# Performance work log

Measured on AMD Instinct MI355X. Metric: run time of the kernel, lower is better.

Reference implementation:

```python
import jax, jax.numpy as jnp
import numpy as np

DIM = 4096
HEADS = 32
HD = DIM // HEADS  # 128
SEQ = 2048
BSZ = 2
ALEN = 10
ROPE_THETA = 10000.0


def _make_freqs(seq, hd):
    inv = 1.0 / (ROPE_THETA ** (np.arange(0, hd, 2, dtype=np.float32) / hd))
    t = np.arange(seq, dtype=np.float32)
    ang = np.outer(t, inv)  # [seq, hd/2]
    return jnp.asarray(np.cos(ang)), jnp.asarray(np.sin(ang))


def setup_inputs() -> dict:
    key = jax.random.key(0)
    ks = jax.random.split(key, 8)
    s = 1.0 / np.sqrt(DIM)
    x = jax.random.normal(ks[0], (BSZ, SEQ, DIM), jnp.float32)
    wq = jax.random.normal(ks[1], (DIM, DIM), jnp.float32) * s  # [in, out]
    wk = jax.random.normal(ks[2], (DIM, DIM), jnp.float32) * s
    wv = jax.random.normal(ks[3], (DIM, DIM), jnp.float32) * s
    wo = jax.random.normal(ks[4], (DIM, DIM), jnp.float32) * s
    gate = 0.1 * jax.random.normal(ks[5], (1, HEADS, 1, 1), jnp.float32)
    adapter = jax.random.normal(ks[6], (1, ALEN, DIM), jnp.float32)
    freqs_cos, freqs_sin = _make_freqs(SEQ, HD)
    # causal additive mask, start_pos = 0
    mask = jnp.triu(jnp.full((1, 1, SEQ, SEQ), -1e9, jnp.float32), k=1)
    return {"x": x, "wq": wq, "wk": wk, "wv": wv, "wo": wo, "gate": gate,
            "adapter": adapter, "freqs_cos": freqs_cos, "freqs_sin": freqs_sin,
            "mask": mask, "start_pos": 0, "random_init": 0}


def _rope(t, cos, sin):
    # t: [b, s, H, hd]; cos/sin: [s, hd/2] -> broadcast (1, s, 1, hd/2)
    b, s, h, hd = t.shape
    t2 = t.reshape(b, s, h, hd // 2, 2)
    tr, ti = t2[..., 0], t2[..., 1]
    c = cos[None, :, None, :]
    sn = sin[None, :, None, :]
    orr = tr * c - ti * sn
    oi = tr * sn + ti * c
    return jnp.stack([orr, oi], axis=-1).reshape(b, s, h, hd)


def reference(x, wq, wk, wv, wo, gate, adapter, freqs_cos, freqs_sin, mask,
              start_pos, random_init):
    bsz, seqlen, dim = x.shape
    hd = 2 * freqs_cos.shape[-1]
    H = dim // hd
    L = adapter.shape[1]
    scale = 1.0 / jnp.sqrt(jnp.float32(hd))

    xq = (x @ wq).reshape(bsz, seqlen, H, hd)
    xk = (x @ wk).reshape(bsz, seqlen, H, hd)
    xv = (x @ wv).reshape(bsz, seqlen, H, hd)

    xq = _rope(xq, freqs_cos, freqs_sin)
    xk = _rope(xk, freqs_cos, freqs_sin)

    # adapter prefix K/V (no RoPE), shared across batch
    ak = (adapter @ wk).reshape(1, L, H, hd)  # [1, L, H, hd]
    av = (adapter @ wv).reshape(1, L, H, hd)

    # scores: normal keys masked causally; adapter keys unmasked (extra zeros)
    scores_n = jnp.einsum('bqhd,bkhd->bhqk', xq, xk) * scale + mask
    scores_a = jnp.einsum('bqhd,lhd->bhql', xq, ak[0]) * scale

    if random_init:
        # joint softmax over [adapter | normal] keys
        sc = jax.nn.softmax(jnp.concatenate([scores_a, scores_n], axis=-1), axis=-1)
        pa, pn = sc[..., :L], sc[..., L:]
    else:
        pa = jnp.tanh(gate) * jax.nn.softmax(scores_a, axis=-1)
        pn = jax.nn.softmax(scores_n, axis=-1)

    out = (jnp.einsum('bhql,lhd->bqhd', pa, av[0])
           + jnp.einsum('bhqk,bkhd->bqhd', pn, xv))
    out = out.reshape(bsz, seqlen, H * hd)
    return out @ wo
```

## Files before the change

### kernel.cpp

```cpp
#include <hip/hip_runtime.h>
#include <hip/hip_bf16.h>
#include <cstdint>

typedef float  f32x4  __attribute__((ext_vector_type(4)));
typedef __bf16 bf16x8 __attribute__((ext_vector_type(8)));
typedef __bf16 bf16x4 __attribute__((ext_vector_type(4)));
typedef __bf16 bf16x2 __attribute__((ext_vector_type(2)));

#define AS1 __attribute__((address_space(1)))
#define AS3 __attribute__((address_space(3)))

static constexpr int D   = 4096;
static constexpr int SEQ = 2048;
static constexpr int MX  = 4224;

__device__ __forceinline__ void gload_lds16(const void* g, void* l) {
  __builtin_amdgcn_global_load_lds((AS1 void*)(g), (AS3 void*)(l), 16, 0, 0);
}

__device__ __forceinline__ f32x4 mfma16(bf16x8 a, bf16x8 b, f32x4 c) {
  return __builtin_amdgcn_mfma_f32_16x16x32_bf16(a, b, c, 0, 0, 0);
}

__device__ __forceinline__ int xcd_chunk(int orig, int nwg) {
  int q = nwg >> 3, r = nwg & 7;
  int xcd = orig & 7, pos = orig >> 3;
  return (xcd < r ? xcd * (q + 1) : r * (q + 1) + (xcd - r) * q) + pos;
}

#define BARF() asm volatile("s_barrier" ::: "memory")

__global__ __launch_bounds__(256) void transpose_cast(const float* __restrict__ W,
                                                      __bf16* __restrict__ WT) {
  __shared__ float tile[64][65];
  const int t  = threadIdx.x;
  const int r0 = blockIdx.x * 64;
  const int c0 = blockIdx.y * 64;
#pragma unroll
  for (int p = 0; p < 4; ++p) {
    int e = p * 1024 + t * 4;
    int row = e >> 6, col = e & 63;
    f32x4 v = *(const f32x4*)(W + (size_t)(r0 + row) * D + c0 + col);
#pragma unroll
    for (int i = 0; i < 4; ++i) tile[row][col + i] = v[i];
  }
  __syncthreads();
#pragma unroll
  for (int p = 0; p < 2; ++p) {
    int e = p * 2048 + t * 8;
    int orow = e >> 6, ocol = e & 63;
    bf16x8 o;
#pragma unroll
    for (int i = 0; i < 8; ++i) o[i] = (__bf16)tile[ocol + i][orow];
    *(bf16x8*)(WT + (size_t)(c0 + orow) * D + r0 + ocol) = o;
  }
}

__global__ __launch_bounds__(256) void build_xa(const float* __restrict__ x,
                                                const float* __restrict__ ad,
                                                __bf16* __restrict__ xa) {
  int idx = blockIdx.x * 256 + threadIdx.x;
  int e = idx * 4;
  int row = e >> 12, col = e & 4095;
  f32x4 v = {};
  if (row < 4096)      v = *(const f32x4*)(x + (size_t)row * D + col);
  else if (row < 4106) v = *(const f32x4*)(ad + (size_t)(row - 4096) * D + col);
  bf16x4 o;
#pragma unroll
  for (int i = 0; i < 4; ++i) o[i] = (__bf16)v[i];
  *(bf16x4*)(xa + (size_t)row * D + col) = o;
}

template <int MODE>
__global__ __launch_bounds__(512, 2) void gemm256(const __bf16* __restrict__ A,
                                                  const __bf16* __restrict__ BT,
                                                  void* __restrict__ O0,
                                                  void* __restrict__ O1,
                                                  void* __restrict__ O2,
                                                  int Mt) {
  __shared__ __bf16 lds[65536];
  const int tid = threadIdx.x;
  const int wv = tid >> 6, ln = tid & 63;
  const int lg = ln >> 4, lr = ln & 15;

  const int nwg = gridDim.x;
  const int wgid = xcd_chunk(blockIdx.x, nwg);
  const int m0 = (wgid % Mt) * 256;
  const int n0 = (wgid / Mt) * 256;

  const int wm = (wv >> 2) * 128, wn = (wv & 3) * 64;

  auto stage = [&](int t) {
    const int buf = t & 1;
    const int kt = t * 64;
#pragma unroll
    for (int i = 0; i < 8; ++i) {
      int c = i * 512 + tid;
      int mat = c >> 11;
      int cm = c & 2047;
      int r = cm >> 3;
      int ch = (cm & 7) ^ (r & 7);
      const __bf16* src = mat ? (BT + (size_t)(n0 + r) * 4096 + kt + ch * 8)
                              : (A  + (size_t)(m0 + r) * 4096 + kt + ch * 8);
      int base = buf * 32768 + mat * 16384 + ((i * 512 + wv * 64) & 2047) * 8;
      gload_lds16(src, lds + base);
    }
  };

  f32x4 acc[8][4] = {};
  bf16x8 aLo[4][2], aHi[4][2], bLo[2][2], bHi[2][2];

  stage(0);

  for (int t = 0; t < 64; ++t) {
    const int buf = t & 1;
    if (t + 1 < 64) {
      stage(t + 1);
      asm volatile("s_waitcnt vmcnt(8)" ::: "memory");
    } else {
      asm volatile("s_waitcnt vmcnt(0)" ::: "memory");
    }
    BARF();

    const __bf16* pA = lds + buf * 32768;
    const __bf16* pB = lds + buf * 32768 + 16384;

    auto rdA = [&](int mi, int kk) -> bf16x8 {
      int r = wm + mi * 16 + lr;
      int R = r & 127;
      int cw = (kk * 4 + lg) ^ (R & 7);
      return *(const bf16x8*)(pA + (r >> 7) * 8192 + R * 64 + cw * 8);
    };
    auto rdB = [&](int ni, int kk) -> bf16x8 {
      int n = wn + ni * 16 + lr;
      int R = n & 127;
      int cw = (kk * 4 + lg) ^ (R & 7);
      return *(const bf16x8*)(pB + (n >> 7) * 8192 + R * 64 + cw * 8);
    };

#pragma unroll
    for (int mi = 0; mi < 4; ++mi)
#pragma unroll
      for (int kk = 0; kk < 2; ++kk) aLo[mi][kk] = rdA(mi, kk);
#pragma unroll
    for (int ni = 0; ni < 2; ++ni)
#pragma unroll
      for (int kk = 0; kk < 2; ++kk) bLo[ni][kk] = rdB(ni, kk);
    BARF();
    __builtin_amdgcn_s_setprio(1);
#pragma unroll
    for (int kk = 0; kk < 2; ++kk)
#pragma unroll
      for (int mi = 0; mi < 4; ++mi)
#pragma unroll
        for (int ni = 0; ni < 2; ++ni)
          acc[mi][ni] = mfma16(aLo[mi][kk], bLo[ni][kk], acc[mi][ni]);
    __builtin_amdgcn_s_setprio(0);

#pragma unroll
    for (int mi = 0; mi < 4; ++mi)
#pragma unroll
      for (int kk = 0; kk < 2; ++kk) aHi[mi][kk] = rdA(mi + 4, kk);
    BARF();
    __builtin_amdgcn_s_setprio(1);
#pragma unroll
    for (int kk = 0; kk < 2; ++kk)
#pragma unroll
      for (int mi = 0; mi < 4; ++mi)
#pragma unroll
        for (int ni = 0; ni < 2; ++ni)
          acc[mi + 4][ni] = mfma16(aHi[mi][kk], bLo[ni][kk], acc[mi + 4][ni]);
    __builtin_amdgcn_s_setprio(0);

#pragma unroll
    for (int ni = 0; ni < 2; ++ni)
#pragma unroll
      for (int kk = 0; kk < 2; ++kk) bHi[ni][kk] = rdB(ni + 2, kk);
    BARF();
    __builtin_amdgcn_s_setprio(1);
#pragma unroll
    for (int kk = 0; kk < 2; ++kk)
#pragma unroll
      for (int mi = 0; mi < 4; ++mi)
#pragma unroll
        for (int ni = 0; ni < 2; ++ni)
          acc[mi + 4][ni + 2] = mfma16(aHi[mi][kk], bHi[ni][kk], acc[mi + 4][ni + 2]);
    __builtin_amdgcn_s_setprio(0);

#pragma unroll
    for (int mi = 0; mi < 4; ++mi)
#pragma unroll
      for (int kk = 0; kk < 2; ++kk) aLo[mi][kk] = rdA(mi, kk);
    BARF();
    __builtin_amdgcn_s_setprio(1);
#pragma unroll
    for (int kk = 0; kk < 2; ++kk)
#pragma unroll
      for (int mi = 0; mi < 4; ++mi)
#pragma unroll
        for (int ni = 0; ni < 2; ++ni)
          acc[mi][ni + 2] = mfma16(aLo[mi][kk], bHi[ni][kk], acc[mi][ni + 2]);
    __builtin_amdgcn_s_setprio(0);

    BARF();
  }

  if constexpr (MODE == 0) {
    const int sel = n0 >> 12;
    __bf16* out = (sel == 0) ? (__bf16*)O0 : (sel == 1) ? (__bf16*)O1 : (__bf16*)O2;
    const int colb = n0 & 4095;
    const int Mmax = (sel == 0) ? 4096 : 4224;
#pragma unroll
    for (int mi = 0; mi < 8; ++mi)
#pragma unroll
      for (int j = 0; j < 4; ++j) {
        int row = m0 + wm + mi * 16 + lg * 4 + j;
        if (row < Mmax) {
#pragma unroll
          for (int ni = 0; ni < 4; ++ni) {
            int col = colb + wn + ni * 16 + lr;
            out[(size_t)row * 4096 + col] = (__bf16)acc[mi][ni][j];
          }
        }
      }
  } else {
    float* out = (float*)O0;
#pragma unroll
    for (int mi = 0; mi < 8; ++mi)
#pragma unroll
      for (int ni = 0; ni < 4; ++ni)
#pragma unroll
        for (int j = 0; j < 4; ++j) {
          int row = m0 + wm + mi * 16 + lg * 4 + j;
          int col = n0 + wn + ni * 16 + lr;
          out[(size_t)row * 4096 + col] = acc[mi][ni][j];
        }
  }
}

__global__ __launch_bounds__(256) void rope_kernel(__bf16* __restrict__ q,
                                                   __bf16* __restrict__ k,
                                                   const float* __restrict__ fc,
                                                   const float* __restrict__ fs) {
  int row = blockIdx.x;
  __bf16* buf = blockIdx.y ? k : q;
  int t = threadIdx.x;
  int s = row & (SEQ - 1);
  int jb = (t & 7) * 8;
  const float* cp = fc + s * 64 + jb;
  const float* sp = fs + s * 64 + jb;
  __bf16* p = buf + (size_t)row * D + t * 16;
  bf16x8 v0 = *(const bf16x8*)p;
  bf16x8 v1 = *(const bf16x8*)(p + 8);
  bf16x8 o0, o1;
#pragma unroll
  for (int i = 0; i < 4; ++i) {
    float C = cp[i], Sn = sp[i];
    float re = (float)v0[2 * i], im = (float)v0[2 * i + 1];
    o0[2 * i]     = (__bf16)(re * C - im * Sn);
    o0[2 * i + 1] = (__bf16)(re * Sn + im * C);
  }
#pragma unroll
  for (int i = 0; i < 4; ++i) {
    float C = cp[4 + i], Sn = sp[4 + i];
    float re = (float)v1[2 * i], im = (float)v1[2 * i + 1];
    o1[2 * i]     = (__bf16)(re * C - im * Sn);
    o1[2 * i + 1] = (__bf16)(re * Sn + im * C);
  }
  *(bf16x8*)p = o0;
  *(bf16x8*)(p + 8) = o1;
}

__global__ __launch_bounds__(256) void transpose_v(const __bf16* __restrict__ V,
                                                   __bf16* __restrict__ VT) {
  __shared__ __bf16 tile[64][72];
  const int t  = threadIdx.x;
  const int r0 = blockIdx.x * 64;
  const int c0 = blockIdx.y * 64;
#pragma unroll
  for (int p = 0; p < 2; ++p) {
    int e = p * 2048 + t * 8;
    int row = e >> 6, col = e & 63;
    bf16x8 v8 = *(const bf16x8*)(V + (size_t)(r0 + row) * D + c0 + col);
#pragma unroll
    for (int i = 0; i < 8; ++i) tile[row][col + i] = v8[i];
  }
  __syncthreads();
#pragma unroll
  for (int p = 0; p < 2; ++p) {
    int e = p * 2048 + t * 8;
    int orow = e >> 6, ocol = e & 63;
    bf16x8 o;
#pragma unroll
    for (int i = 0; i < 8; ++i) o[i] = tile[ocol + i][orow];
    *(bf16x8*)(VT + (size_t)(c0 + orow) * MX + r0 + ocol) = o;
  }
}

__global__ __launch_bounds__(256) void attn_kernel(const __bf16* __restrict__ Q,
                                                   const __bf16* __restrict__ K,
                                                   const __bf16* __restrict__ VT,
                                                   const float* __restrict__ gate,
                                                   __bf16* __restrict__ Out) {
  __shared__ __bf16 Ks[2][64 * 128];
  __shared__ __bf16 Vs[2][128 * 64];
  __shared__ __bf16 Ps[4][32 * 64];

  const int tid = threadIdx.x;
  const int wv = tid >> 6, ln = tid & 63;
  const int lg = ln >> 4, lr = ln & 15;

  const int wgid = xcd_chunk(blockIdx.x, 512);
  const int px = wgid & 7;
  const int hb = wgid >> 3;
  const int h = hb & 31, b = hb >> 5;

  const float scale = 0.08838834764831845f;
  const float g = tanhf(gate[h]);

  auto stage = [&](int t, int buf) {
    const int kv0 = t * 64;
#pragma unroll
    for (int j = 0; j < 4; ++j) {
      int c = wv * 256 + j * 64 + ln;
      int rk = c >> 4, sck = (c & 15) ^ (rk & 7);
      gload_lds16(K + (size_t)(b * SEQ + kv0 + rk) * D + h * 128 + sck * 8,
                  Ks[buf] + (wv * 256 + j * 64) * 8);
      int rv = c >> 3, scv = (c & 7) ^ (rv & 7);
      gload_lds16(VT + (size_t)(h * 128 + rv) * MX + b * SEQ + kv0 + scv * 8,
                  Vs[buf] + (wv * 256 + j * 64) * 8);
    }
  };

  auto run_supertile = [&](int qt) {
    const int q0 = qt * 128;
    const int qbase = b * SEQ + q0 + wv * 32;

    bf16x8 qf[2][4];
#pragma unroll
    for (int mi = 0; mi < 2; ++mi)
#pragma unroll
      for (int kd = 0; kd < 4; ++kd)
        qf[mi][kd] = *(const bf16x8*)(Q + (size_t)(qbase + mi * 16 + lr) * D +
                                      h * 128 + kd * 32 + lg * 8);

    f32x4 O[2][8] = {};
    float mI2[2], lI2[2];
#pragma unroll
    for (int mi = 0; mi < 2; ++mi) { mI2[mi] = -1e30f; lI2[mi] = 0.f; }

    const int ntiles = 2 * qt + 2;
    stage(0, 0);

    for (int t = 0; t < ntiles; ++t) {
      const int cur = t & 1;
      const int kv0 = t * 64;
      if (t + 1 < ntiles) {
        stage(t + 1, cur ^ 1);
        asm volatile("s_waitcnt vmcnt(8)" ::: "memory");
      } else {
        asm volatile("s_waitcnt vmcnt(0)" ::: "memory");
      }
      __builtin_amdgcn_s_barrier();
      __builtin_amdgcn_sched_barrier(0);

      f32x4 S[2][4] = {};
      __builtin_amdgcn_s_setprio(1);
#pragma unroll
      for (int kd = 0; kd < 4; ++kd) {
        bf16x8 kf[4];
#pragma unroll
        for (int nf = 0; nf < 4; ++nf) {
          int kr = nf * 16 + lr;
          kf[nf] = *(const bf16x8*)(Ks[cur] + kr * 128 +
                                    (((kd * 4 + lg) ^ (kr & 7)) * 8));
        }
#pragma unroll
        for (int mi = 0; mi < 2; ++mi)
#pragma unroll
          for (int nf = 0; nf < 4; ++nf)
            S[mi][nf] = mfma16(kf[nf], qf[mi][kd], S[mi][nf]);
      }
      __builtin_amdgcn_s_setprio(0);

      float r2[2]; int grew = 0;
#pragma unroll
      for (int mi = 0; mi < 2; ++mi) {
        const int qg = q0 + wv * 32 + mi * 16 + lr;
        float mo = mI2[mi];
        float mt = -3e38f;
#pragma unroll
        for (int nf = 0; nf < 4; ++nf)
#pragma unroll
          for (int j = 0; j < 4; ++j) {
            int kvg = kv0 + nf * 16 + lg * 4 + j;
            float s = S[mi][nf][j] * scale;
            s = (kvg > qg) ? -1e30f : s;
            S[mi][nf][j] = s;
            mt = fmaxf(mt, s);
          }
        mt = fmaxf(mt, __shfl_xor(mt, 16));
        mt = fmaxf(mt, __shfl_xor(mt, 32));
        float mn = fmaxf(mo, mt);
        float ps = 0.f;
#pragma unroll
        for (int nf = 0; nf < 4; ++nf)
#pragma unroll
          for (int j = 0; j < 4; ++j) {
            float p = __expf(S[mi][nf][j] - mn);
            S[mi][nf][j] = p;
            ps += p;
          }
        ps += __shfl_xor(ps, 16);
        ps += __shfl_xor(ps, 32);
        float r = __expf(mo - mn);
        lI2[mi] = lI2[mi] * r + ps;
        mI2[mi] = mn;
        r2[mi] = r;
        grew |= (mn > mo) ? 1 : 0;
      }
      if (__any(grew)) {
#pragma unroll
        for (int mi = 0; mi < 2; ++mi)
#pragma unroll
          for (int j = 0; j < 4; ++j) {
            float rj = __shfl(r2[mi], lg * 4 + j);
#pragma unroll
            for (int n = 0; n < 8; ++n) O[mi][n][j] *= rj;
          }
      }

#pragma unroll
      for (int mi = 0; mi < 2; ++mi) {
        int q = mi * 16 + lr;
#pragma unroll
        for (int nf = 0; nf < 4; ++nf)
#pragma unroll
          for (int jj = 0; jj < 2; ++jj) {
            int kv = nf * 16 + lg * 4 + 2 * jj;
            bf16x2 pk;
            pk[0] = (__bf16)S[mi][nf][2 * jj];
            pk[1] = (__bf16)S[mi][nf][2 * jj + 1];
            *(bf16x2*)(Ps[wv] + q * 64 + (((kv >> 3) ^ (q & 7)) * 8) + (kv & 7)) = pk;
          }
      }

      __builtin_amdgcn_s_setprio(1);
#pragma unroll
      for (int kkv = 0; kkv < 2; ++kkv) {
        bf16x8 pf[2];
#pragma unroll
        for (int mi = 0; mi < 2; ++mi) {
          int prw = mi * 16 + lr;
          pf[mi] = *(const bf16x8*)(Ps[wv] + prw * 64 +
                                    (((kkv * 4 + lg) ^ (prw & 7)) * 8));
        }
#pragma unroll
        for (int n = 0; n < 8; ++n) {
          int vr = n * 16 + lr;
          bf16x8 vf = *(const bf16x8*)(Vs[cur] + vr * 64 +
                                       (((kkv * 4 + lg) ^ (vr & 7)) * 8));
#pragma unroll
          for (int mi = 0; mi < 2; ++mi) O[mi][n] = mfma16(pf[mi], vf, O[mi][n]);
        }
      }
      __builtin_amdgcn_s_setprio(0);

      __builtin_amdgcn_s_barrier();
      __builtin_amdgcn_sched_barrier(0);
    }

#pragma unroll
    for (int mi = 0; mi < 2; ++mi) {
      float inv = 1.0f / lI2[mi];
#pragma unroll
      for (int j = 0; j < 4; ++j) {
        float invj = __shfl(inv, lg * 4 + j);
#pragma unroll
        for (int n = 0; n < 8; ++n) O[mi][n][j] *= invj;
      }
    }

    {
      f32x4 Sa[2] = {};
#pragma unroll
      for (int kd = 0; kd < 4; ++kd) {
        bf16x8 kfa = *(const bf16x8*)(K + (size_t)(2 * SEQ + lr) * D +
                                      h * 128 + kd * 32 + lg * 8);
#pragma unroll
        for (int mi = 0; mi < 2; ++mi) Sa[mi] = mfma16(kfa, qf[mi][kd], Sa[mi]);
      }
#pragma unroll
      for (int mi = 0; mi < 2; ++mi) {
        float mt = -3e38f;
#pragma unroll
        for (int j = 0; j < 4; ++j) {
          int kv = lg * 4 + j;
          float s = Sa[mi][j] * scale;
          s = (kv >= 10) ? -1e30f : s;
          Sa[mi][j] = s;
          mt = fmaxf(mt, s);
        }
        mt = fmaxf(mt, __shfl_xor(mt, 16));
        mt = fmaxf(mt, __shfl_xor(mt, 32));
        float ps = 0.f;
#pragma unroll
        for (int j = 0; j < 4; ++j) {
          float p = __expf(Sa[mi][j] - mt);
          Sa[mi][j] = p;
          ps += p;
        }
        ps += __shfl_xor(ps, 16);
        ps += __shfl_xor(ps, 32);
        float gs = g / ps;
        int q = mi * 16 + lr;
#pragma unroll
        for (int jj = 0; jj < 2; ++jj) {
          int kv = lg * 4 + 2 * jj;
          bf16x2 pk;
          pk[0] = (__bf16)(Sa[mi][2 * jj] * gs);
          pk[1] = (__bf16)(Sa[mi][2 * jj + 1] * gs);
          *(bf16x2*)(Ps[wv] + q * 64 + (((kv >> 3) ^ (q & 7)) * 8) + (kv & 7)) = pk;
          int kv2 = 16 + kv;
          bf16x2 z = {};
          *(bf16x2*)(Ps[wv] + q * 64 + (((kv2 >> 3) ^ (q & 7)) * 8) + (kv2 & 7)) = z;
        }
      }
      bf16x8 pfa[2];
#pragma unroll
      for (int mi = 0; mi < 2; ++mi) {
        int prw = mi * 16 + lr;
        pfa[mi] = *(const bf16x8*)(Ps[wv] + prw * 64 + ((lg ^ (prw & 7)) * 8));
      }
#pragma unroll
      for (int n = 0; n < 8; ++n) {
        bf16x8 vfa = *(const bf16x8*)(VT + (size_t)(h * 128 + n * 16 + lr) * MX +
                                      2 * SEQ + lg * 8);
#pragma unroll
        for (int mi = 0; mi < 2; ++mi) O[mi][n] = mfma16(pfa[mi], vfa, O[mi][n]);
      }
    }

#pragma unroll
    for (int mi = 0; mi < 2; ++mi)
#pragma unroll
      for (int n = 0; n < 8; ++n)
#pragma unroll
        for (int j = 0; j < 4; ++j)
          Out[(size_t)(qbase + mi * 16 + lg * 4 + j) * D + h * 128 + n * 16 + lr] =
              (__bf16)O[mi][n][j];
  };

  run_supertile(15 - px);
  run_supertile(px);
}

extern "C" void kernel_launch(void* const* d_in, const int* in_sizes, int n_in,
                              void* d_out, int out_size, void* d_ws, size_t ws_size,
                              hipStream_t stream) {
  const float* x    = (const float*)d_in[0];
  const float* wq   = (const float*)d_in[1];
  const float* wk   = (const float*)d_in[2];
  const float* wv   = (const float*)d_in[3];
  const float* wo   = (const float*)d_in[4];
  const float* gate = (const float*)d_in[5];
  const float* ad   = (const float*)d_in[6];
  const float* fc   = (const float*)d_in[7];
  const float* fs   = (const float*)d_in[8];

  const size_t WSZ = (size_t)D * D * 2;
  const size_t XSZ = (size_t)MX * D * 2;
  if (ws_size < 4 * WSZ + XSZ + WSZ + 3 * XSZ) return;

  char* w = (char*)d_ws;
  size_t off = 0;
  auto alloc = [&](size_t sz) { void* p = w + off; off += sz; return p; };
  __bf16* wqT = (__bf16*)alloc(WSZ);
  __bf16* wkT = (__bf16*)alloc(WSZ);
  __bf16* wvT = (__bf16*)alloc(WSZ);
  __bf16* woT = (__bf16*)alloc(WSZ);
  __bf16* xa  = (__bf16*)alloc(XSZ);
  __bf16* qb  = (__bf16*)alloc(WSZ);
  __bf16* kb  = (__bf16*)alloc(XSZ);
  __bf16* vb  = (__bf16*)alloc(XSZ);
  __bf16* vT  = (__bf16*)alloc(XSZ);
  __bf16* attn = vb;

  dim3 blk(256);
  transpose_cast<<<dim3(64, 64), blk, 0, stream>>>(wq, wqT);
  transpose_cast<<<dim3(64, 64), blk, 0, stream>>>(wk, wkT);
  transpose_cast<<<dim3(64, 64), blk, 0, stream>>>(wv, wvT);
  transpose_cast<<<dim3(64, 64), blk, 0, stream>>>(wo, woT);
  build_xa<<<dim3(16896), blk, 0, stream>>>(x, ad, xa);

  gemm256<0><<<dim3(17 * 48), dim3(512), 0, stream>>>(xa, wqT, qb, kb, vb, 17);

  rope_kernel<<<dim3(4096, 2), blk, 0, stream>>>(qb, kb, fc, fs);
  transpose_v<<<dim3(66, 64), blk, 0, stream>>>(vb, vT);

  attn_kernel<<<dim3(512), blk, 0, stream>>>(qb, kb, vT, gate, attn);

  gemm256<1><<<dim3(16 * 16), dim3(512), 0, stream>>>(attn, woT, d_out, nullptr, nullptr, 16);
}
```

Before: 913.0 us.

## Split GEMM prefetch into quarter stages and move adapter rows to separate kernel

```diff
diff --git a/kernel.cpp b/kernel.cpp
--- a/kernel.cpp
+++ b/kernel.cpp
@@ -87,43 +87,37 @@
   const int wgid = xcd_chunk(blockIdx.x, nwg);
   const int m0 = (wgid % Mt) * 256;
   const int n0 = (wgid / Mt) * 256;
-
   const int wm = (wv >> 2) * 128, wn = (wv & 3) * 64;
 
-  auto stage = [&](int t) {
-    const int buf = t & 1;
-    const int kt = t * 64;
-#pragma unroll
-    for (int i = 0; i < 8; ++i) {
+  auto stageHalf = [&](int k, int mat, int half) {
+    const int slot = k & 1;
+    const int kt = k * 64;
+    const __bf16* base = mat ? BT + (size_t)(n0 + half * 128) * 4096
+                             : A  + (size_t)(m0 + half * 128) * 4096;
+#pragma unroll
+    for (int i = 0; i < 2; ++i) {
       int c = i * 512 + tid;
-      int mat = c >> 11;
-      int cm = c & 2047;
-      int r = cm >> 3;
-      int ch = (cm & 7) ^ (r & 7);
-      const __bf16* src = mat ? (BT + (size_t)(n0 + r) * 4096 + kt + ch * 8)
-                              : (A  + (size_t)(m0 + r) * 4096 + kt + ch * 8);
-      int base = buf * 32768 + mat * 16384 + ((i * 512 + wv * 64) & 2047) * 8;
-      gload_lds16(src, lds + base);
+      int r = c >> 3;
+      int ch = (c & 7) ^ (r & 7);
+      gload_lds16(base + (size_t)r * 4096 + kt + ch * 8,
+                  lds + slot * 32768 + mat * 16384 + half * 8192 +
+                      (i * 512 + wv * 64) * 8);
     }
   };
 
   f32x4 acc[8][4] = {};
   bf16x8 aLo[4][2], aHi[4][2], bLo[2][2], bHi[2][2];
 
-  stage(0);
-
-  for (int t = 0; t < 64; ++t) {
-    const int buf = t & 1;
-    if (t + 1 < 64) {
-      stage(t + 1);
-      asm volatile("s_waitcnt vmcnt(8)" ::: "memory");
-    } else {
-      asm volatile("s_waitcnt vmcnt(0)" ::: "memory");
-    }
-    BARF();
-
-    const __bf16* pA = lds + buf * 32768;
-    const __bf16* pB = lds + buf * 32768 + 16384;
+  stageHalf(0, 0, 0);
+  stageHalf(0, 1, 0);
+  stageHalf(0, 0, 1);
+  stageHalf(0, 1, 1);
+
+  for (int k = 0; k < 64; ++k) {
+    const int slot = k & 1;
+    const __bf16* pA = lds + slot * 32768;
+    const __bf16* pB = lds + slot * 32768 + 16384;
+    const bool pf = (k + 1 < 64);
 
     auto rdA = [&](int mi, int kk) -> bf16x8 {
       int r = wm + mi * 16 + lr;
@@ -138,6 +132,10 @@
       return *(const bf16x8*)(pB + (n >> 7) * 8192 + R * 64 + cw * 8);
     };
 
+    if (pf) stageHalf(k + 1, 0, 0);
+    if (pf) asm volatile("s_waitcnt vmcnt(2)" ::: "memory");
+    else    asm volatile("s_waitcnt vmcnt(0)" ::: "memory");
+    BARF();
 #pragma unroll
     for (int mi = 0; mi < 4; ++mi)
 #pragma unroll
@@ -146,7 +144,6 @@
     for (int ni = 0; ni < 2; ++ni)
 #pragma unroll
       for (int kk = 0; kk < 2; ++kk) bLo[ni][kk] = rdB(ni, kk);
-    BARF();
     __builtin_amdgcn_s_setprio(1);
 #pragma unroll
     for (int kk = 0; kk < 2; ++kk)
@@ -156,7 +153,9 @@
         for (int ni = 0; ni < 2; ++ni)
           acc[mi][ni] = mfma16(aLo[mi][kk], bLo[ni][kk], acc[mi][ni]);
     __builtin_amdgcn_s_setprio(0);
-
+    BARF();
+
+    if (pf) stageHalf(k + 1, 1, 0);
 #pragma unroll
     for (int mi = 0; mi < 4; ++mi)
 #pragma unroll
@@ -171,7 +170,9 @@
         for (int ni = 0; ni < 2; ++ni)
           acc[mi + 4][ni] = mfma16(aHi[mi][kk], bLo[ni][kk], acc[mi + 4][ni]);
     __builtin_amdgcn_s_setprio(0);
-
+    BARF();
+
+    if (pf) stageHalf(k + 1, 0, 1);
 #pragma unroll
     for (int ni = 0; ni < 2; ++ni)
 #pragma unroll
@@ -186,7 +187,9 @@
         for (int ni = 0; ni < 2; ++ni)
           acc[mi + 4][ni + 2] = mfma16(aHi[mi][kk], bHi[ni][kk], acc[mi + 4][ni + 2]);
     __builtin_amdgcn_s_setprio(0);
-
+    BARF();
+
+    if (pf) stageHalf(k + 1, 1, 1);
 #pragma unroll
     for (int mi = 0; mi < 4; ++mi)
 #pragma unroll
@@ -201,7 +204,6 @@
         for (int ni = 0; ni < 2; ++ni)
           acc[mi][ni + 2] = mfma16(aLo[mi][kk], bHi[ni][kk], acc[mi][ni + 2]);
     __builtin_amdgcn_s_setprio(0);
-
     BARF();
   }
 
@@ -209,20 +211,16 @@
     const int sel = n0 >> 12;
     __bf16* out = (sel == 0) ? (__bf16*)O0 : (sel == 1) ? (__bf16*)O1 : (__bf16*)O2;
     const int colb = n0 & 4095;
-    const int Mmax = (sel == 0) ? 4096 : 4224;
 #pragma unroll
     for (int mi = 0; mi < 8; ++mi)
 #pragma unroll
-      for (int j = 0; j < 4; ++j) {
-        int row = m0 + wm + mi * 16 + lg * 4 + j;
-        if (row < Mmax) {
-#pragma unroll
-          for (int ni = 0; ni < 4; ++ni) {
-            int col = colb + wn + ni * 16 + lr;
-            out[(size_t)row * 4096 + col] = (__bf16)acc[mi][ni][j];
-          }
-        }
-      }
+      for (int ni = 0; ni < 4; ++ni)
+#pragma unroll
+        for (int j = 0; j < 4; ++j) {
+          int row = m0 + wm + mi * 16 + lg * 4 + j;
+          int col = colb + wn + ni * 16 + lr;
+          out[(size_t)row * 4096 + col] = (__bf16)acc[mi][ni][j];
+        }
   } else {
     float* out = (float*)O0;
 #pragma unroll
@@ -236,6 +234,35 @@
           out[(size_t)row * 4096 + col] = acc[mi][ni][j];
         }
   }
+}
+
+__global__ __launch_bounds__(256) void gemm_adapter(const __bf16* __restrict__ xa,
+                                                    const __bf16* __restrict__ BT,
+                                                    __bf16* __restrict__ kb,
+                                                    __bf16* __restrict__ vb) {
+  const int tid = threadIdx.x;
+  const int wv = tid >> 6, ln = tid & 63;
+  const int lg = ln >> 4, lr = ln & 15;
+  const int col0 = blockIdx.x * 256 + wv * 64;
+  f32x4 acc[4] = {};
+  for (int kt = 0; kt < 4096; kt += 32) {
+    bf16x8 a = *(const bf16x8*)(xa + (size_t)(4096 + lr) * 4096 + kt + lg * 8);
+#pragma unroll
+    for (int ni = 0; ni < 4; ++ni) {
+      bf16x8 b = *(const bf16x8*)(BT + (size_t)(col0 + ni * 16 + lr) * 4096 +
+                                  kt + lg * 8);
+      acc[ni] = mfma16(a, b, acc[ni]);
+    }
+  }
+#pragma unroll
+  for (int ni = 0; ni < 4; ++ni)
+#pragma unroll
+    for (int j = 0; j < 4; ++j) {
+      int row = 4096 + lg * 4 + j;
+      int col = col0 + ni * 16 + lr;
+      __bf16* out = (col < 4096) ? kb : vb;
+      out[(size_t)row * 4096 + (col & 4095)] = (__bf16)acc[ni][j];
+    }
 }
 
 __global__ __launch_bounds__(256) void rope_kernel(__bf16* __restrict__ q,
@@ -593,7 +620,8 @@
   transpose_cast<<<dim3(64, 64), blk, 0, stream>>>(wo, woT);
   build_xa<<<dim3(16896), blk, 0, stream>>>(x, ad, xa);
 
-  gemm256<0><<<dim3(17 * 48), dim3(512), 0, stream>>>(xa, wqT, qb, kb, vb, 17);
+  gemm256<0><<<dim3(16 * 48), dim3(512), 0, stream>>>(xa, wqT, qb, kb, vb, 16);
+  gemm_adapter<<<dim3(32), blk, 0, stream>>>(xa, wkT, kb, vb);
 
   rope_kernel<<<dim3(4096, 2), blk, 0, stream>>>(qb, kb, fc, fs);
   transpose_v<<<dim3(66, 64), blk, 0, stream>>>(vb, vT);
```

Measured after the change: 898.0 us. About the same (-1.6%).
